# Kernel tuning notes

Hardware: AMD Instinct MI355X
Metric: run time of the kernel (lower is better)

Reference implementation:

```python
import jax, jax.numpy as jnp
import numpy as np

B, S, D_IN, D_H, D_OUT, NB = 4, 4096, 1024, 1024, 1024, 8
BD = D_H // NB  # block size of the block-diagonal gate projections
R_MIN, R_MAX, EPS = 0.9, 0.999, 1e-8


def setup_inputs() -> dict:
    key = jax.random.key(0)
    ks = jax.random.split(key, 8)
    x = jax.random.normal(ks[0], (B, S, D_IN), dtype=jnp.float32)
    h0 = jnp.zeros((B, D_H), dtype=jnp.float32)
    # input projection Dense(d_hidden)
    W_in = jax.random.normal(ks[1], (D_IN, D_H), dtype=jnp.float32) / np.sqrt(D_IN)
    b_in = jnp.zeros((D_H,), dtype=jnp.float32)
    # two BlockDiagonalLinear gate projections (n_blocks blocks of [BD, BD])
    Wgx = jax.random.normal(ks[2], (NB, BD, BD), dtype=jnp.float32) / np.sqrt(BD)
    bgx = jnp.zeros((D_H,), dtype=jnp.float32)
    Wga = jax.random.normal(ks[3], (NB, BD, BD), dtype=jnp.float32) / np.sqrt(BD)
    bga = jnp.zeros((D_H,), dtype=jnp.float32)
    # stable_init_real: softplus(param) == -log(r) with r ~ U[r_min, r_max] in magnitude
    u = jax.random.uniform(ks[4], (D_H,), dtype=jnp.float32)
    a_real = 0.5 * jnp.log(u * (R_MAX**2 - R_MIN**2) + R_MIN**2 + EPS)
    a_real_param = jnp.log(jnp.exp(-a_real) - 1.0)
    # output projection Dense(d_out)
    W_out = jax.random.normal(ks[5], (D_H, D_OUT), dtype=jnp.float32) / np.sqrt(D_H)
    b_out = jnp.zeros((D_OUT,), dtype=jnp.float32)
    return dict(x=x, h0=h0, W_in=W_in, b_in=b_in, Wgx=Wgx, bgx=bgx,
                Wga=Wga, bga=bga, a_real_param=a_real_param,
                W_out=W_out, b_out=b_out)


def _block_diag_linear(x, W, b):
    # x: [B,S,D_H] -> split into NB blocks of BD, per-block matmul
    xb = x.reshape(x.shape[0], x.shape[1], NB, BD)
    y = jnp.einsum('bsni,nio->bsno', xb, W)
    return y.reshape(x.shape[0], x.shape[1], D_H) + b


def reference(x, h0, W_in, b_in, Wgx, bgx, Wga, bga, a_real_param, W_out, b_out):
    # input projection
    x = x @ W_in + b_in  # [B,S,D_H]
    # input-dependent gates (sigmoid of block-diagonal projections)
    gate_x = jax.nn.sigmoid(_block_diag_linear(x, Wgx, bgx))
    gate_a = jax.nn.sigmoid(_block_diag_linear(x, Wga, bga))
    # real-only RG-LRU recurrence coefficient: a = exp(-8 * gate_a * softplus(c))
    log_a = -8.0 * gate_a * jax.nn.softplus(a_real_param)  # [B,S,D_H], <= 0
    a = jnp.exp(log_a)
    # gated input with sqrt(1 - a^2) normalization (sqrt_bound_derivative fwd == sqrt)
    gx = gate_x * x * jnp.sqrt(1.0 - jnp.exp(2.0 * log_a))
    # fold initial state into the first step: h_1 = a_1 * h0 + gx_1
    gx = gx.at[:, 0].add(a[:, 0] * h0)
    # linear scan h_t = a_t * h_{t-1} + gx_t via associative scan over seq axis
    def combine(c1, c2):
        a1, x1 = c1
        a2, x2 = c2
        return (a2 * a1, a2 * x1 + x2)
    _, h = jax.lax.associative_scan(combine, (a, gx), axis=1)  # [B,S,D_H]
    out = h @ W_out + b_out  # [B,S,D_OUT]
    return out, h[:, -1]
```

## Files before the change

kernel.cpp:

```cpp
#include <hip/hip_runtime.h>

#define B_SZ 4
#define SEQ 4096
#define DIN 1024
#define DH 1024
#define DOUT 1024
#define NBLK 8
#define MTOK (B_SZ * SEQ)
#define CHUNK 64
#define NCHUNK (SEQ / CHUNK)

typedef _Float16 half8 __attribute__((ext_vector_type(8)));
typedef _Float16 half4v __attribute__((ext_vector_type(4)));
typedef float f32x4 __attribute__((ext_vector_type(4)));

union HPack { unsigned int u; _Float16 h[2]; };

__device__ __forceinline__ void gl_lds16(const void* g, void* l) {
  __builtin_amdgcn_global_load_lds((__attribute__((address_space(1))) void*)g,
                                   (__attribute__((address_space(3))) void*)l,
                                   16, 0, 0);
}

__device__ __forceinline__ void bar_fence() {
  asm volatile("" ::: "memory");
  __builtin_amdgcn_s_barrier();
  asm volatile("" ::: "memory");
}

__device__ __forceinline__ int swz_h(int r, int c) {
  return (((r << 8) | (c << 1)) ^ ((r & 7) << 4)) >> 1;
}

__global__ __launch_bounds__(256)
void prep_kernel(const float* __restrict__ x, _Float16* __restrict__ x_h,
                 const float* __restrict__ Win, const float* __restrict__ Wout,
                 const float* __restrict__ Wgx, const float* __restrict__ Wga,
                 _Float16* __restrict__ WinT, _Float16* __restrict__ WoutT,
                 _Float16* __restrict__ WgxT, _Float16* __restrict__ WgaT) {
  __shared__ float tile[64][65];
  if (blockIdx.x < 16384) {
    const int gid = blockIdx.x * 256 + threadIdx.x;
    const float4 v = ((const float4*)x)[gid];
    half4v h;
    h[0] = (_Float16)v.x; h[1] = (_Float16)v.y; h[2] = (_Float16)v.z; h[3] = (_Float16)v.w;
    ((half4v*)x_h)[gid] = h;
    return;
  }
  int t = blockIdx.x - 16384;
  const float* src; _Float16* dst; int C; size_t bo = 0;
  if (t < 256)      { src = Win;  dst = WinT;  C = 1024; }
  else if (t < 512) { src = Wout; dst = WoutT; C = 1024; t -= 256; }
  else if (t < 544) { int u = t - 512; src = Wgx; dst = WgxT; C = 128;
                      bo = (size_t)(u >> 2) * (128 * 128); t = u & 3; }
  else              { int u = t - 544; src = Wga; dst = WgaT; C = 128;
                      bo = (size_t)(u >> 2) * (128 * 128); t = u & 3; }
  const int nbx = C >> 6;
  const int r0 = (t / nbx) * 64, c0 = (t % nbx) * 64;
  const int tr = threadIdx.x >> 6, tc = threadIdx.x & 63;
#pragma unroll
  for (int i = 0; i < 64; i += 4)
    tile[tr + i][tc] = src[bo + (size_t)(r0 + tr + i) * C + c0 + tc];
  __syncthreads();
#pragma unroll
  for (int i = 0; i < 64; i += 4) {
    const int cc = i + tr;
    dst[bo + (size_t)(c0 + cc) * C + r0 + tc] = (_Float16)tile[tc][cc];
  }
}

template <int OUT_F32>
__global__ __launch_bounds__(256, 4)
void gemm_bt(const _Float16* __restrict__ A, const _Float16* __restrict__ Bt,
             const float* __restrict__ bias, void* __restrict__ C,
             int M, int N, int K) {
  __shared__ __align__(16) _Float16 smem[16384];
  const int tid = threadIdx.x;
  const int wave = tid >> 6, lane = tid & 63;
  const int n0 = blockIdx.x * 128, m0 = blockIdx.y * 128;
  const int wm = (wave >> 1) * 64, wn = (wave & 1) * 64;
  const int row = lane & 15, quad = lane >> 4;
  const int srow = lane >> 2;
  const int ssl  = ((lane & 3) ^ (srow & 3)) * 8;
  const int sslot = (quad ^ (row & 3)) * 8;

  auto stage = [&](int kt, int buf) {
#pragma unroll
    for (int ci = 0; ci < 2; ci++) {
      const int c = wave * 2 + ci;
      gl_lds16(A  + (size_t)(m0 + c * 16 + srow) * K + kt + ssl, smem + buf + c * 512);
      gl_lds16(Bt + (size_t)(n0 + c * 16 + srow) * K + kt + ssl, smem + 8192 + buf + c * 512);
    }
  };

  f32x4 acc[4][4] = {};
  stage(0, 0);
  stage(32, 4096);
  asm volatile("s_waitcnt vmcnt(4)" ::: "memory");
  bar_fence();

  const int nt = K >> 5;
  int co = 0;
#pragma unroll 1
  for (int t = 0; t < nt; ++t) {
    half8 af[4], bf[4];
#pragma unroll
    for (int i = 0; i < 4; i++)
      af[i] = *(const half8*)&smem[co + (wm + i * 16 + row) * 32 + sslot];
#pragma unroll
    for (int j = 0; j < 4; j++)
      bf[j] = *(const half8*)&smem[8192 + co + (wn + j * 16 + row) * 32 + sslot];
#pragma unroll
    for (int i = 0; i < 4; i++)
#pragma unroll
      for (int j = 0; j < 4; j++)
        acc[i][j] = __builtin_amdgcn_mfma_f32_16x16x32_f16(af[i], bf[j], acc[i][j], 0, 0, 0);
    bar_fence();
    if (t + 2 < nt) {
      stage((t + 2) * 32, co);
      asm volatile("s_waitcnt vmcnt(4)" ::: "memory");
    } else {
      asm volatile("s_waitcnt vmcnt(0)" ::: "memory");
    }
    bar_fence();
    co ^= 4096;
  }

  float bv[4];
#pragma unroll
  for (int j = 0; j < 4; j++) bv[j] = bias[n0 + wn + j * 16 + row];
#pragma unroll
  for (int i = 0; i < 4; i++) {
#pragma unroll
    for (int r = 0; r < 4; r++) {
      const int m = m0 + wm + i * 16 + quad * 4 + r;
      const size_t base = (size_t)m * N + n0 + wn + row;
#pragma unroll
      for (int j = 0; j < 4; j++) {
        const float v = acc[i][j][r] + bv[j];
        if (OUT_F32) ((float*)C)[base + j * 16] = v;
        else         ((_Float16*)C)[base + j * 16] = (_Float16)v;
      }
    }
  }
}

__global__ __launch_bounds__(256, 4)
void gemm1_gates(const _Float16* __restrict__ A, const _Float16* __restrict__ Bt,
                 const float* __restrict__ bias,
                 const _Float16* __restrict__ WxT, const _Float16* __restrict__ WaT,
                 const float* __restrict__ bgx, const float* __restrict__ bga,
                 const float* __restrict__ arp,
                 unsigned int* __restrict__ ag,
                 float* __restrict__ cA, float* __restrict__ cH) {
  __shared__ __align__(16) _Float16 smem[16384];
  const int tid = threadIdx.x;
  const int wave = tid >> 6, lane = tid & 63;
  const int nb = blockIdx.x, n0 = nb * 128, m0 = blockIdx.y * 128;
  const int wm = (wave >> 1) * 64, wn = (wave & 1) * 64;
  const int row = lane & 15, quad = lane >> 4;
  const int srow = lane >> 2;
  const int ssl  = ((lane & 3) ^ (srow & 3)) * 8;
  const int sslot = (quad ^ (row & 3)) * 8;

  auto stage = [&](int kt, int buf) {
#pragma unroll
    for (int ci = 0; ci < 2; ci++) {
      const int c = wave * 2 + ci;
      gl_lds16(A  + (size_t)(m0 + c * 16 + srow) * DIN + kt + ssl, smem + buf + c * 512);
      gl_lds16(Bt + (size_t)(n0 + c * 16 + srow) * DIN + kt + ssl, smem + 8192 + buf + c * 512);
    }
  };

  f32x4 acc[4][4] = {};
  stage(0, 0);
  stage(32, 4096);
  asm volatile("s_waitcnt vmcnt(4)" ::: "memory");
  bar_fence();

  const int nt = DIN >> 5;
  int co = 0;
#pragma unroll 1
  for (int t = 0; t < nt; ++t) {
    half8 af[4], bf[4];
#pragma unroll
    for (int i = 0; i < 4; i++)
      af[i] = *(const half8*)&smem[co + (wm + i * 16 + row) * 32 + sslot];
#pragma unroll
    for (int j = 0; j < 4; j++)
      bf[j] = *(const half8*)&smem[8192 + co + (wn + j * 16 + row) * 32 + sslot];
#pragma unroll
    for (int i = 0; i < 4; i++)
#pragma unroll
      for (int j = 0; j < 4; j++)
        acc[i][j] = __builtin_amdgcn_mfma_f32_16x16x32_f16(af[i], bf[j], acc[i][j], 0, 0, 0);
    bar_fence();
    if (t + 2 < nt) {
      stage((t + 2) * 32, co);
      asm volatile("s_waitcnt vmcnt(4)" ::: "memory");
    } else {
      asm volatile("s_waitcnt vmcnt(0)" ::: "memory");
    }
    bar_fence();
    co ^= 4096;
  }

  {
    float bv[4];
#pragma unroll
    for (int j = 0; j < 4; j++) bv[j] = bias[n0 + wn + j * 16 + row];
#pragma unroll
    for (int i = 0; i < 4; i++)
#pragma unroll
      for (int r = 0; r < 4; r++) {
        const int tl = wm + i * 16 + quad * 4 + r;
#pragma unroll
        for (int j = 0; j < 4; j++)
          smem[swz_h(tl, wn + j * 16 + row)] = (_Float16)(acc[i][j][r] + bv[j]);
      }
  }
  __syncthreads();

  const _Float16* const WxB = WxT + (size_t)nb * (128 * 128);
  const _Float16* const WaB = WaT + (size_t)nb * (128 * 128);
  const int b_idx = (m0 + wm) >> 12;
  const int c_idx = ((m0 + wm) & (SEQ - 1)) >> 6;
  const int cbase = c_idx * (B_SZ * DH) + b_idx * DH + n0 + wn + row;
  const size_t agbase = ((size_t)(blockIdx.y * NBLK + nb) * 4 + wave) * 4096;

#pragma unroll 1
  for (int jp = 0; jp < 2; jp++) {
    f32x4 accx[4][2] = {}, acca[4][2] = {};
#pragma unroll
    for (int kk = 0; kk < 128; kk += 32) {
      half8 af[4];
#pragma unroll
      for (int i = 0; i < 4; i++)
        af[i] = *(const half8*)&smem[swz_h(wm + i * 16 + row, kk + quad * 8)];
#pragma unroll
      for (int jj = 0; jj < 2; jj++) {
        const size_t wo = (size_t)(wn + (jp * 2 + jj) * 16 + row) * 128 + kk + quad * 8;
        const half8 bx = *(const half8*)&WxB[wo];
        const half8 ba = *(const half8*)&WaB[wo];
#pragma unroll
        for (int i = 0; i < 4; i++) {
          accx[i][jj] = __builtin_amdgcn_mfma_f32_16x16x32_f16(af[i], bx, accx[i][jj], 0, 0, 0);
          acca[i][jj] = __builtin_amdgcn_mfma_f32_16x16x32_f16(af[i], ba, acca[i][jj], 0, 0, 0);
        }
      }
    }
    float bxv[2], bav[2], cd[2];
#pragma unroll
    for (int jj = 0; jj < 2; jj++) {
      const int d = n0 + wn + (jp * 2 + jj) * 16 + row;
      bxv[jj] = bgx[d]; bav[jj] = bga[d];
      cd[jj] = log1pf(expf(arp[d]));
    }
    float Arun[2] = {1.f, 1.f}, Hrun[2] = {0.f, 0.f};
#pragma unroll
    for (int i = 0; i < 4; i++) {
      float Aseg[2] = {1.f, 1.f}, Hseg[2] = {0.f, 0.f};
#pragma unroll
      for (int r = 0; r < 4; r++) {
        const int tl = wm + i * 16 + quad * 4 + r;
#pragma unroll
        for (int jj = 0; jj < 2; jj++) {
          const float px = accx[i][jj][r] + bxv[jj];
          const float pa = acca[i][jj][r] + bav[jj];
          const float sx = 1.f / (1.f + __expf(-px));
          const float sa = 1.f / (1.f + __expf(-pa));
          const float a = __expf(-8.f * sa * cd[jj]);
          const float n2 = fmaxf(1.f - a * a, 0.f);
          const float xv = (float)smem[swz_h(tl, wn + (jp * 2 + jj) * 16 + row)];
          HPack pk;
          pk.h[0] = (_Float16)a;
          pk.h[1] = (_Float16)(sx * xv * sqrtf(n2));
          ag[agbase + (size_t)(((i * 4 + r) * 4) + jp * 2 + jj) * 64 + lane] = pk.u;
          const float ar = (float)pk.h[0], gr = (float)pk.h[1];
          Aseg[jj] *= ar;
          Hseg[jj] = fmaf(ar, Hseg[jj], gr);
        }
      }
#pragma unroll
      for (int jj = 0; jj < 2; jj++) {
        float A1 = Aseg[jj], H1 = Hseg[jj];
        float A2 = __shfl_down(A1, 16, 64), H2 = __shfl_down(H1, 16, 64);
        H1 = fmaf(A2, H1, H2); A1 *= A2;
        A2 = __shfl_down(A1, 32, 64); H2 = __shfl_down(H1, 32, 64);
        H1 = fmaf(A2, H1, H2); A1 *= A2;
        Hrun[jj] = fmaf(A1, Hrun[jj], H1);
        Arun[jj] *= A1;
      }
    }
    if (lane < 16) {
#pragma unroll
      for (int jj = 0; jj < 2; jj++) {
        cA[cbase + (jp * 2 + jj) * 16] = Arun[jj];
        cH[cbase + (jp * 2 + jj) * 16] = Hrun[jj];
      }
    }
  }
}

__global__ __launch_bounds__(256)
void scan_p2(const float* __restrict__ cA, const float* __restrict__ cH,
             const float* __restrict__ h0, float* __restrict__ cin,
             float* __restrict__ hlast) {
  const int wave = threadIdx.x >> 6, lane = threadIdx.x & 63;
  const int g = blockIdx.x * 4 + wave;
  float A = cA[(size_t)lane * (B_SZ * DH) + g], H = cH[(size_t)lane * (B_SZ * DH) + g];
#pragma unroll
  for (int d = 1; d < 64; d <<= 1) {
    const float Ap = __shfl_up(A, d, 64), Hp = __shfl_up(H, d, 64);
    if (lane >= d) { H = fmaf(A, Hp, H); A *= Ap; }
  }
  const float h0g = h0[g];
  if (lane == 63) hlast[g] = fmaf(A, h0g, H);
  float Ae = __shfl_up(A, 1, 64), He = __shfl_up(H, 1, 64);
  if (lane == 0) { Ae = 1.f; He = 0.f; }
  cin[(size_t)lane * (B_SZ * DH) + g] = fmaf(Ae, h0g, He);
}

__global__ __launch_bounds__(256)
void scan_p3(const unsigned int* __restrict__ ag,
             const float* __restrict__ cin, _Float16* __restrict__ h) {
  const int gtid = blockIdx.x * 256 + threadIdx.x;
  const int d = gtid & (DH - 1);
  const int bc = gtid >> 10;
  const int b = bc >> 6, c = bc & (NCHUNK - 1);
  const int mblk = b * 32 + (c >> 1), wmb = c & 1;
  const int nb = d >> 7, wnb = (d >> 6) & 1, j = (d >> 4) & 3, row = d & 15;
  const size_t agb = ((size_t)(mblk * NBLK + nb) * 4 + wmb * 2 + wnb) * 4096
                   + j * 64 + row;
  const size_t hbase = ((size_t)(b * SEQ + c * CHUNK)) * DH + d;
  float carry = cin[c * (B_SZ * DH) + b * DH + d];
#pragma unroll 8
  for (int t = 0; t < CHUNK; t++) {
    HPack pk;
    pk.u = ag[agb + (size_t)(((t >> 4) * 4 + (t & 3)) * 4) * 64 + ((t >> 2) & 3) * 16];
    const float av = (float)pk.h[0];
    const float gv = (float)pk.h[1];
    carry = fmaf(av, carry, gv);
    h[hbase + (size_t)t * DH] = (_Float16)carry;
  }
}

extern "C" void kernel_launch(void* const* d_in, const int* in_sizes, int n_in,
                              void* d_out, int out_size, void* d_ws, size_t ws_size,
                              hipStream_t stream) {
  const float* x     = (const float*)d_in[0];
  const float* h0    = (const float*)d_in[1];
  const float* W_in  = (const float*)d_in[2];
  const float* b_in  = (const float*)d_in[3];
  const float* Wgx   = (const float*)d_in[4];
  const float* bgx   = (const float*)d_in[5];
  const float* Wga   = (const float*)d_in[6];
  const float* bga   = (const float*)d_in[7];
  const float* arp   = (const float*)d_in[8];
  const float* W_out = (const float*)d_in[9];
  const float* b_out = (const float*)d_in[10];
  float* out = (float*)d_out;
  float* hlast = out + (size_t)MTOK * DOUT;

  char* p = (char*)d_ws;
  auto take = [&](size_t bytes) { char* r = p; p += (bytes + 255) & ~(size_t)255; return r; };
  _Float16* x_h   = (_Float16*)take((size_t)MTOK * DIN * 2);
  unsigned int* ag = (unsigned int*)take((size_t)MTOK * DH * 4);
  _Float16* WinT  = (_Float16*)take((size_t)DIN * DH * 2);
  _Float16* WoutT = (_Float16*)take((size_t)DH * DOUT * 2);
  _Float16* WgxT  = (_Float16*)take((size_t)NBLK * 128 * 128 * 2);
  _Float16* WgaT  = (_Float16*)take((size_t)NBLK * 128 * 128 * 2);
  float* cA   = (float*)take((size_t)NCHUNK * B_SZ * DH * 4);
  float* cH   = (float*)take((size_t)NCHUNK * B_SZ * DH * 4);
  float* cin  = (float*)take((size_t)NCHUNK * B_SZ * DH * 4);
  _Float16* h_buf = x_h;

  prep_kernel<<<16384 + 576, 256, 0, stream>>>(x, x_h, W_in, W_out, Wgx, Wga,
                                               WinT, WoutT, WgxT, WgaT);
  gemm1_gates<<<dim3(NBLK, MTOK / 128), 256, 0, stream>>>(
      x_h, WinT, b_in, WgxT, WgaT, bgx, bga, arp, ag, cA, cH);
  scan_p2<<<(B_SZ * DH) / 4, 256, 0, stream>>>(cA, cH, h0, cin, hlast);
  scan_p3<<<(B_SZ * NCHUNK * DH) / 256, 256, 0, stream>>>(ag, cin, h_buf);
  gemm_bt<1><<<dim3(DOUT / 128, MTOK / 128), 256, 0, stream>>>(h_buf, WoutT, b_out, out, MTOK, DOUT, DH);
}
```

Measured before the change: 313.0 us.

## Fuse x fp32-to-fp16 conversion into gemm1 load path and swap grid order

Removes the separate pass that converts x from fp32 to fp16 in the prep kernel. gemm1 now loads x as fp32 into registers, converts it, and writes it to LDS inside a manually double-buffered pipeline, while B still goes through global_load_lds. This drops a 64MB read plus 32MB write round trip of x_h, at the cost of register-staged A loads and twice the A bytes read per tile. Both GEMMs also swap their grid so that M varies along blockIdx.x, which changes how tiles reuse data in L2.

```diff
diff --git a/kernel.cpp b/kernel.cpp
--- a/kernel.cpp
+++ b/kernel.cpp
@@ -33,21 +33,12 @@
 }
 
 __global__ __launch_bounds__(256)
-void prep_kernel(const float* __restrict__ x, _Float16* __restrict__ x_h,
-                 const float* __restrict__ Win, const float* __restrict__ Wout,
+void prep_kernel(const float* __restrict__ Win, const float* __restrict__ Wout,
                  const float* __restrict__ Wgx, const float* __restrict__ Wga,
                  _Float16* __restrict__ WinT, _Float16* __restrict__ WoutT,
                  _Float16* __restrict__ WgxT, _Float16* __restrict__ WgaT) {
   __shared__ float tile[64][65];
-  if (blockIdx.x < 16384) {
-    const int gid = blockIdx.x * 256 + threadIdx.x;
-    const float4 v = ((const float4*)x)[gid];
-    half4v h;
-    h[0] = (_Float16)v.x; h[1] = (_Float16)v.y; h[2] = (_Float16)v.z; h[3] = (_Float16)v.w;
-    ((half4v*)x_h)[gid] = h;
-    return;
-  }
-  int t = blockIdx.x - 16384;
+  int t = blockIdx.x;
   const float* src; _Float16* dst; int C; size_t bo = 0;
   if (t < 256)      { src = Win;  dst = WinT;  C = 1024; }
   else if (t < 512) { src = Wout; dst = WoutT; C = 1024; t -= 256; }
@@ -77,7 +68,7 @@
   __shared__ __align__(16) _Float16 smem[16384];
   const int tid = threadIdx.x;
   const int wave = tid >> 6, lane = tid & 63;
-  const int n0 = blockIdx.x * 128, m0 = blockIdx.y * 128;
+  const int m0 = blockIdx.x * 128, n0 = blockIdx.y * 128;
   const int wm = (wave >> 1) * 64, wn = (wave & 1) * 64;
   const int row = lane & 15, quad = lane >> 4;
   const int srow = lane >> 2;
@@ -146,7 +137,7 @@
 }
 
 __global__ __launch_bounds__(256, 4)
-void gemm1_gates(const _Float16* __restrict__ A, const _Float16* __restrict__ Bt,
+void gemm1_gates(const float* __restrict__ Ax, const _Float16* __restrict__ Bt,
                  const float* __restrict__ bias,
                  const _Float16* __restrict__ WxT, const _Float16* __restrict__ WaT,
                  const float* __restrict__ bgx, const float* __restrict__ bga,
@@ -156,54 +147,108 @@
   __shared__ __align__(16) _Float16 smem[16384];
   const int tid = threadIdx.x;
   const int wave = tid >> 6, lane = tid & 63;
-  const int nb = blockIdx.x, n0 = nb * 128, m0 = blockIdx.y * 128;
+  const int m0 = blockIdx.x * 128, nb = blockIdx.y, n0 = nb * 128;
   const int wm = (wave >> 1) * 64, wn = (wave & 1) * 64;
   const int row = lane & 15, quad = lane >> 4;
   const int srow = lane >> 2;
   const int ssl  = ((lane & 3) ^ (srow & 3)) * 8;
   const int sslot = (quad ^ (row & 3)) * 8;
-
-  auto stage = [&](int kt, int buf) {
-#pragma unroll
-    for (int ci = 0; ci < 2; ci++) {
-      const int c = wave * 2 + ci;
-      gl_lds16(A  + (size_t)(m0 + c * 16 + srow) * DIN + kt + ssl, smem + buf + c * 512);
-      gl_lds16(Bt + (size_t)(n0 + c * 16 + srow) * DIN + kt + ssl, smem + 8192 + buf + c * 512);
-    }
+  const int c0 = wave * 2, c1 = c0 + 1;
+  const float* a0p = Ax + (size_t)(m0 + c0 * 16 + srow) * DIN + ssl;
+  const float* a1p = Ax + (size_t)(m0 + c1 * 16 + srow) * DIN + ssl;
+  const _Float16* b0p = Bt + (size_t)(n0 + c0 * 16 + srow) * DIN + ssl;
+  const _Float16* b1p = Bt + (size_t)(n0 + c1 * 16 + srow) * DIN + ssl;
+  _Float16* const wA0 = smem + c0 * 512 + lane * 8;
+  _Float16* const wA1 = smem + c1 * 512 + lane * 8;
+
+  auto cvt8 = [](float4 u, float4 v) {
+    half8 h;
+    h[0] = (_Float16)u.x; h[1] = (_Float16)u.y; h[2] = (_Float16)u.z; h[3] = (_Float16)u.w;
+    h[4] = (_Float16)v.x; h[5] = (_Float16)v.y; h[6] = (_Float16)v.z; h[7] = (_Float16)v.w;
+    return h;
   };
 
   f32x4 acc[4][4] = {};
-  stage(0, 0);
-  stage(32, 4096);
-  asm volatile("s_waitcnt vmcnt(4)" ::: "memory");
+  float4 ra0, ra1, ra2, ra3, rb0, rb1, rb2, rb3;
+  ra0 = *(const float4*)(a0p + 0);  ra1 = *(const float4*)(a0p + 4);
+  ra2 = *(const float4*)(a1p + 0);  ra3 = *(const float4*)(a1p + 4);
+  gl_lds16(b0p + 0, smem + 8192 + c0 * 512);
+  gl_lds16(b1p + 0, smem + 8192 + c1 * 512);
+  asm volatile("s_waitcnt vmcnt(0)" ::: "memory");
+  *(half8*)wA0 = cvt8(ra0, ra1);
+  *(half8*)wA1 = cvt8(ra2, ra3);
+  rb0 = *(const float4*)(a0p + 32); rb1 = *(const float4*)(a0p + 36);
+  rb2 = *(const float4*)(a1p + 32); rb3 = *(const float4*)(a1p + 36);
+  gl_lds16(b0p + 32, smem + 8192 + 4096 + c0 * 512);
+  gl_lds16(b1p + 32, smem + 8192 + 4096 + c1 * 512);
+  asm volatile("s_waitcnt lgkmcnt(0)" ::: "memory");
   bar_fence();
 
   const int nt = DIN >> 5;
-  int co = 0;
 #pragma unroll 1
-  for (int t = 0; t < nt; ++t) {
-    half8 af[4], bf[4];
-#pragma unroll
-    for (int i = 0; i < 4; i++)
-      af[i] = *(const half8*)&smem[co + (wm + i * 16 + row) * 32 + sslot];
-#pragma unroll
-    for (int j = 0; j < 4; j++)
-      bf[j] = *(const half8*)&smem[8192 + co + (wn + j * 16 + row) * 32 + sslot];
-#pragma unroll
-    for (int i = 0; i < 4; i++)
+  for (int t = 0; t < nt; t += 2) {
+    {
+      half8 af[4], bf[4];
+#pragma unroll
+      for (int i = 0; i < 4; i++)
+        af[i] = *(const half8*)&smem[(wm + i * 16 + row) * 32 + sslot];
 #pragma unroll
       for (int j = 0; j < 4; j++)
-        acc[i][j] = __builtin_amdgcn_mfma_f32_16x16x32_f16(af[i], bf[j], acc[i][j], 0, 0, 0);
+        bf[j] = *(const half8*)&smem[8192 + (wn + j * 16 + row) * 32 + sslot];
+#pragma unroll
+      for (int i = 0; i < 4; i++)
+#pragma unroll
+        for (int j = 0; j < 4; j++)
+          acc[i][j] = __builtin_amdgcn_mfma_f32_16x16x32_f16(af[i], bf[j], acc[i][j], 0, 0, 0);
+    }
     bar_fence();
     if (t + 2 < nt) {
-      stage((t + 2) * 32, co);
-      asm volatile("s_waitcnt vmcnt(4)" ::: "memory");
+      const int k2 = (t + 2) * 32;
+      ra0 = *(const float4*)(a0p + k2);  ra1 = *(const float4*)(a0p + k2 + 4);
+      ra2 = *(const float4*)(a1p + k2);  ra3 = *(const float4*)(a1p + k2 + 4);
+      gl_lds16(b0p + k2, smem + 8192 + c0 * 512);
+      gl_lds16(b1p + k2, smem + 8192 + c1 * 512);
+      asm volatile("s_waitcnt vmcnt(6)" ::: "memory");
     } else {
       asm volatile("s_waitcnt vmcnt(0)" ::: "memory");
     }
-    bar_fence();
-    co ^= 4096;
-  }
+    *(half8*)(wA0 + 4096) = cvt8(rb0, rb1);
+    *(half8*)(wA1 + 4096) = cvt8(rb2, rb3);
+    asm volatile("s_waitcnt lgkmcnt(0)" ::: "memory");
+    bar_fence();
+    {
+      half8 af[4], bf[4];
+#pragma unroll
+      for (int i = 0; i < 4; i++)
+        af[i] = *(const half8*)&smem[4096 + (wm + i * 16 + row) * 32 + sslot];
+#pragma unroll
+      for (int j = 0; j < 4; j++)
+        bf[j] = *(const half8*)&smem[8192 + 4096 + (wn + j * 16 + row) * 32 + sslot];
+#pragma unroll
+      for (int i = 0; i < 4; i++)
+#pragma unroll
+        for (int j = 0; j < 4; j++)
+          acc[i][j] = __builtin_amdgcn_mfma_f32_16x16x32_f16(af[i], bf[j], acc[i][j], 0, 0, 0);
+    }
+    bar_fence();
+    if (t + 3 < nt) {
+      const int k3 = (t + 3) * 32;
+      rb0 = *(const float4*)(a0p + k3);  rb1 = *(const float4*)(a0p + k3 + 4);
+      rb2 = *(const float4*)(a1p + k3);  rb3 = *(const float4*)(a1p + k3 + 4);
+      gl_lds16(b0p + k3, smem + 8192 + 4096 + c0 * 512);
+      gl_lds16(b1p + k3, smem + 8192 + 4096 + c1 * 512);
+      asm volatile("s_waitcnt vmcnt(6)" ::: "memory");
+    } else {
+      asm volatile("s_waitcnt vmcnt(0)" ::: "memory");
+    }
+    if (t + 2 < nt) {
+      *(half8*)wA0 = cvt8(ra0, ra1);
+      *(half8*)wA1 = cvt8(ra2, ra3);
+    }
+    asm volatile("s_waitcnt lgkmcnt(0)" ::: "memory");
+    bar_fence();
+  }
+  __syncthreads();
 
   {
     float bv[4];
@@ -226,7 +271,7 @@
   const int b_idx = (m0 + wm) >> 12;
   const int c_idx = ((m0 + wm) & (SEQ - 1)) >> 6;
   const int cbase = c_idx * (B_SZ * DH) + b_idx * DH + n0 + wn + row;
-  const size_t agbase = ((size_t)(blockIdx.y * NBLK + nb) * 4 + wave) * 4096;
+  const size_t agbase = ((size_t)(blockIdx.x * NBLK + nb) * 4 + wave) * 4096;
 
 #pragma unroll 1
   for (int jp = 0; jp < 2; jp++) {
@@ -364,7 +409,7 @@
 
   char* p = (char*)d_ws;
   auto take = [&](size_t bytes) { char* r = p; p += (bytes + 255) & ~(size_t)255; return r; };
-  _Float16* x_h   = (_Float16*)take((size_t)MTOK * DIN * 2);
+  _Float16* h_buf = (_Float16*)take((size_t)MTOK * DH * 2);
   unsigned int* ag = (unsigned int*)take((size_t)MTOK * DH * 4);
   _Float16* WinT  = (_Float16*)take((size_t)DIN * DH * 2);
   _Float16* WoutT = (_Float16*)take((size_t)DH * DOUT * 2);
@@ -373,13 +418,12 @@
   float* cA   = (float*)take((size_t)NCHUNK * B_SZ * DH * 4);
   float* cH   = (float*)take((size_t)NCHUNK * B_SZ * DH * 4);
   float* cin  = (float*)take((size_t)NCHUNK * B_SZ * DH * 4);
-  _Float16* h_buf = x_h;
-
-  prep_kernel<<<16384 + 576, 256, 0, stream>>>(x, x_h, W_in, W_out, Wgx, Wga,
-                                               WinT, WoutT, WgxT, WgaT);
-  gemm1_gates<<<dim3(NBLK, MTOK / 128), 256, 0, stream>>>(
-      x_h, WinT, b_in, WgxT, WgaT, bgx, bga, arp, ag, cA, cH);
+
+  prep_kernel<<<576, 256, 0, stream>>>(W_in, W_out, Wgx, Wga,
+                                       WinT, WoutT, WgxT, WgaT);
+  gemm1_gates<<<dim3(MTOK / 128, NBLK), 256, 0, stream>>>(
+      x, WinT, b_in, WgxT, WgaT, bgx, bga, arp, ag, cA, cH);
   scan_p2<<<(B_SZ * DH) / 4, 256, 0, stream>>>(cA, cH, h0, cin, hlast);
   scan_p3<<<(B_SZ * NCHUNK * DH) / 256, 256, 0, stream>>>(ag, cin, h_buf);
-  gemm_bt<1><<<dim3(DOUT / 128, MTOK / 128), 256, 0, stream>>>(h_buf, WoutT, b_out, out, MTOK, DOUT, DH);
-}
+  gemm_bt<1><<<dim3(MTOK / 128, DOUT / 128), 256, 0, stream>>>(h_buf, WoutT, b_out, out, MTOK, DOUT, DH);
+}
```

Measured after the change: 386.3 us. +23.4%, slower.
